# Optimization experiments

Hardware: AMD Instinct MI355X
Metric: run time of the kernel (lower is better)

## Reference

```python
import jax, jax.numpy as jnp
import numpy as np

WIN = 7       # window_size (square)
SHIFT = 3     # shift_size
HEADS = 4
WS = WIN * WIN  # 49 tokens per window


def _rel_index():
    # Swin relative position index, shape (WS*WS,), static ints
    coords = np.stack(np.meshgrid(np.arange(WIN), np.arange(WIN), indexing='ij'))
    cf = coords.reshape(2, -1)
    rel = (cf[:, :, None] - cf[:, None, :]).transpose(1, 2, 0)  # (WS, WS, 2)
    rel[:, :, 0] += WIN - 1
    rel[:, :, 1] += WIN - 1
    rel[:, :, 0] *= 2 * WIN - 1
    return rel.sum(-1).reshape(-1)

_REL_IDX = jnp.asarray(_rel_index())


def _attn_mask(H, W):
    # shift mask per window, shape (num_windows, WS, WS), static
    m = np.zeros((H, W), np.float32)
    cnt = 0
    for h in ((0, -WIN), (-WIN, -SHIFT), (-SHIFT, None)):
        for w in ((0, -WIN), (-WIN, -SHIFT), (-SHIFT, None)):
            m[h[0]:h[1], w[0]:w[1]] = cnt
            cnt += 1
    m = m.reshape(H // WIN, WIN, W // WIN, WIN).transpose(0, 2, 1, 3).reshape(-1, WS)
    diff = m[:, None, :] - m[:, :, None]
    return np.where(diff == 0, 0.0, -100.0).astype(np.float32)


def setup_inputs() -> dict:
    key = jax.random.key(0)
    ks = jax.random.split(key, 6)
    C = 128
    return {
        'x': jax.random.normal(ks[0], (64, 56, 56, C), jnp.float32),
        'qkv_kernel': jax.random.normal(ks[1], (C, 3 * C), jnp.float32) * (C ** -0.5),
        'qkv_bias': jax.random.normal(ks[2], (3 * C,), jnp.float32) * 0.02,
        'proj_kernel': jax.random.normal(ks[3], (C, C), jnp.float32) * (C ** -0.5),
        'proj_bias': jax.random.normal(ks[4], (C,), jnp.float32) * 0.02,
        'rel_pos_table': jax.random.normal(ks[5], ((2 * WIN - 1) ** 2, HEADS), jnp.float32) * 0.02,
    }


def reference(x, qkv_kernel, qkv_bias, proj_kernel, proj_bias, rel_pos_table):
    B, H, W, C = x.shape
    nH, nW = H // WIN, W // WIN
    head_dim = C // HEADS

    # cyclic shift + window partition -> (B*nH*nW, WS, C)
    xs = jnp.roll(x, (-SHIFT, -SHIFT), axis=(1, 2))
    xw = xs.reshape(B, nH, WIN, nW, WIN, C).transpose(0, 1, 3, 2, 4, 5).reshape(B * nH * nW, WS, C)

    qkv = xw @ qkv_kernel + qkv_bias
    qkv = qkv.reshape(-1, WS, 3, HEADS, head_dim).transpose(2, 0, 3, 1, 4)  # (3, n, h, WS, d)
    q, k, v = qkv[0], qkv[1], qkv[2]

    attn = jnp.einsum('nhsd,nhtd->nhst', q * head_dim ** -0.5, k)

    # relative position bias: (1, heads, WS, WS)
    bias = rel_pos_table[_REL_IDX].reshape(WS, WS, HEADS).transpose(2, 0, 1)[None]
    attn = attn + bias

    # shift mask (static)
    mask = jnp.asarray(_attn_mask(H, W))  # (nH*nW, WS, WS)
    attn = attn.reshape(B, nH * nW, HEADS, WS, WS) + mask[None, :, None]
    attn = jax.nn.softmax(attn.reshape(-1, HEADS, WS, WS), axis=-1)

    out = jnp.einsum('nhst,nhtd->nhsd', attn, v).transpose(0, 2, 1, 3).reshape(-1, WS, C)
    out = out @ proj_kernel + proj_bias

    # window merge + reverse shift
    out = out.reshape(B, nH, nW, WIN, WIN, C).transpose(0, 1, 3, 2, 4, 5).reshape(B, H, W, C)
    return jnp.roll(out, (SHIFT, SHIFT), axis=(1, 2))
```

## Files before the change

### kernel.cpp

```cpp
#include <hip/hip_runtime.h>
#include <hip/hip_bf16.h>

#define WIN 7
#define SHIFT_SZ 3
#define WSQ 49
#define CH 128
#define HW 56
#define LOG2E 1.4426950408889634f
#define QSCALE (0.17677669529663687f * LOG2E)

typedef short s16x8 __attribute__((ext_vector_type(8)));
typedef short s16x4 __attribute__((ext_vector_type(4)));
typedef float f32x4 __attribute__((ext_vector_type(4)));


__global__ void prep_weights(const float* __restrict__ qkv_kernel,
                             const float* __restrict__ proj_kernel,
                             __hip_bfloat16* __restrict__ ws) {
  int idx = blockIdx.x * 256 + threadIdx.x;
  if (idx < 49152) {
    int n = idx >> 7, c = idx & 127;
    ws[idx] = __float2bfloat16(qkv_kernel[c * 384 + n]);
  }
  if (idx < 16384) {
    int n = idx >> 7, c = idx & 127;
    ws[49152 + idx] = __float2bfloat16(proj_kernel[c * 128 + n]);
  }
}

__global__ void prep_tbl(const float* __restrict__ rel_pos_table,
                         __hip_bfloat16* __restrict__ tbl) {
  int idx = blockIdx.x * 256 + threadIdx.x;
  int t = idx & 63;
  int s = (idx >> 6) & 63;
  int h = (idx >> 12) & 3;
  int cls = idx >> 14;
  float v;
  if (t >= WSQ) v = -43280.f;
  else if (s >= WSQ) v = 0.f;
  else {
    int i1 = s / 7, j1 = s % 7, i2 = t / 7, j2 = t % 7;
    int ridx = (i1 - i2 + 6) * 13 + (j1 - j2 + 6);
    float bias = rel_pos_table[ridx * 4 + h];
    int wyIs7 = cls >> 1, wxIs7 = cls & 1;
    int rh1 = wyIs7 ? (i1 < 4 ? 1 : 2) : 0;
    int rh2 = wyIs7 ? (i2 < 4 ? 1 : 2) : 0;
    int rw1 = wxIs7 ? (j1 < 4 ? 1 : 2) : 0;
    int rw2 = wxIs7 ? (j2 < 4 ? 1 : 2) : 0;
    float mask = (rh1 == rh2 && rw1 == rw2) ? 0.f : -100.f;
    v = (bias + mask) * LOG2E;
  }
  tbl[idx] = __float2bfloat16(v);
}


__launch_bounds__(512, 6)
__global__ void swin_attn(const float* __restrict__ x,
                          const float* __restrict__ qkv_bias,
                          const float* __restrict__ proj_bias,
                          const __hip_bfloat16* __restrict__ wqkvT,
                          const __hip_bfloat16* __restrict__ wprojT,
                          const __hip_bfloat16* __restrict__ tbl,
                          float* __restrict__ out) {
  __shared__ __align__(16) char smem[49152];
  __hip_bfloat16* a_lds  = (__hip_bfloat16*)smem;
  __hip_bfloat16* q_lds  = (__hip_bfloat16*)smem;
  __hip_bfloat16* k_lds  = (__hip_bfloat16*)(smem + 16384);
  __hip_bfloat16* vt_lds = (__hip_bfloat16*)(smem + 32768);
  __hip_bfloat16* p_lds  = (__hip_bfloat16*)smem;
  __hip_bfloat16* o_lds  = (__hip_bfloat16*)(smem + 32768);

  const int tid = threadIdx.x;
  const int lane = tid & 63;
  const int wv = tid >> 6;
  const int g = lane >> 4;
  const int c = lane & 15;
  const int e = c & 7;
  const int e2 = (c >> 1) & 7;

  const int widx = blockIdx.x;
  const int b  = widx >> 6;
  const int wy = (widx >> 3) & 7;
  const int wx = widx & 7;
  const int mc = ((wy == 7) ? 2 : 0) + ((wx == 7) ? 1 : 0);

  for (int it = tid; it < 1024; it += 512) {
    int s = it >> 4;
    int l16 = it & 15;
    union { s16x8 v; __hip_bfloat16 h[8]; } u;
    if (s < WSQ) {
      int i = s / 7, j = s - i * 7;
      int hh = wy * 7 + i + SHIFT_SZ; if (hh >= HW) hh -= HW;
      int ww = wx * 7 + j + SHIFT_SZ; if (ww >= HW) ww -= HW;
      const float4* src = (const float4*)(x + (((b * HW + hh) * HW + ww) * CH + l16 * 8));
      float4 f0 = src[0], f1 = src[1];
      u.h[0] = __float2bfloat16(f0.x); u.h[1] = __float2bfloat16(f0.y);
      u.h[2] = __float2bfloat16(f0.z); u.h[3] = __float2bfloat16(f0.w);
      u.h[4] = __float2bfloat16(f1.x); u.h[5] = __float2bfloat16(f1.y);
      u.h[6] = __float2bfloat16(f1.z); u.h[7] = __float2bfloat16(f1.w);
    } else {
      #pragma unroll
      for (int q = 0; q < 8; ++q) u.h[q] = __float2bfloat16(0.f);
    }
    *(s16x8*)(a_lds + s * 128 + ((l16 ^ (s & 7)) * 8)) = u.v;
  }
  __syncthreads();

  {
    f32x4 acc_v[4];
    #pragma unroll
    for (int mt = 0; mt < 4; ++mt) acc_v[mt] = (f32x4){0.f, 0.f, 0.f, 0.f};
    #pragma unroll
    for (int kt = 0; kt < 4; ++kt) {
      s16x8 bv = *(const s16x8*)(wqkvT + (16 * (16 + wv) + c) * 128 + kt * 32 + g * 8);
      #pragma unroll
      for (int mt = 0; mt < 4; ++mt) {
        s16x8 af = *(const s16x8*)(a_lds + (16 * mt + c) * 128 + ((4 * kt + g) ^ e) * 8);
        acc_v[mt] = __builtin_amdgcn_mfma_f32_16x16x32_bf16(af, bv, acc_v[mt], 0, 0, 0);
      }
    }
    int hv = wv >> 1;
    int d = (wv & 1) * 16 + c;
    float bvb = qkv_bias[256 + wv * 16 + c];
    __hip_bfloat16* vdst = vt_lds + (hv * 32 + d) * 64;
    #pragma unroll
    for (int mt = 0; mt < 4; ++mt) {
      union { s16x4 v; __hip_bfloat16 h[4]; } u;
      #pragma unroll
      for (int r = 0; r < 4; ++r) u.h[r] = __float2bfloat16(acc_v[mt][r] + bvb);
      *(s16x4*)(vdst + ((2 * mt + (g >> 1)) ^ e) * 8 + (g & 1) * 4) = u.v;
    }
  }

  {
    f32x4 acc[2][4];
    #pragma unroll
    for (int ntl = 0; ntl < 2; ++ntl)
      #pragma unroll
      for (int mt = 0; mt < 4; ++mt) acc[ntl][mt] = (f32x4){0.f, 0.f, 0.f, 0.f};
    #pragma unroll
    for (int kt = 0; kt < 4; ++kt) {
      s16x8 af[4];
      #pragma unroll
      for (int mt = 0; mt < 4; ++mt)
        af[mt] = *(const s16x8*)(a_lds + (16 * mt + c) * 128 + ((4 * kt + g) ^ e) * 8);
      #pragma unroll
      for (int ntl = 0; ntl < 2; ++ntl) {
        s16x8 bf = *(const s16x8*)(wqkvT + (16 * (2 * wv + ntl) + c) * 128 + kt * 32 + g * 8);
        #pragma unroll
        for (int mt = 0; mt < 4; ++mt)
          acc[ntl][mt] = __builtin_amdgcn_mfma_f32_16x16x32_bf16(bf, af[mt], acc[ntl][mt], 0, 0, 0);
      }
    }
    const float scale = (wv < 4) ? QSCALE : 1.0f;
    if (wv >= 4) {
      #pragma unroll
      for (int ntl = 0; ntl < 2; ++ntl) {
        int qt = 2 * wv + ntl;
        int h = (qt >> 1) & 3;
        int blk = (qt & 1) * 4 + g;
        float4 b4 = *(const float4*)(qkv_bias + qt * 16 + 4 * g);
        __hip_bfloat16* dst = k_lds + h * 2048;
        #pragma unroll
        for (int mt = 0; mt < 4; ++mt) {
          union { s16x4 v; __hip_bfloat16 h[4]; } u;
          u.h[0] = __float2bfloat16((acc[ntl][mt][0] + b4.x) * scale);
          u.h[1] = __float2bfloat16((acc[ntl][mt][1] + b4.y) * scale);
          u.h[2] = __float2bfloat16((acc[ntl][mt][2] + b4.z) * scale);
          u.h[3] = __float2bfloat16((acc[ntl][mt][3] + b4.w) * scale);
          *(s16x4*)(dst + (16 * mt + c) * 32 + ((blk ^ e2) * 4)) = u.v;
        }
      }
    }
    __syncthreads();
    if (wv < 4) {
      #pragma unroll
      for (int ntl = 0; ntl < 2; ++ntl) {
        int qt = 2 * wv + ntl;
        int h = (qt >> 1) & 3;
        int blk = (qt & 1) * 4 + g;
        float4 b4 = *(const float4*)(qkv_bias + qt * 16 + 4 * g);
        __hip_bfloat16* dst = q_lds + h * 2048;
        #pragma unroll
        for (int mt = 0; mt < 4; ++mt) {
          union { s16x4 v; __hip_bfloat16 h[4]; } u;
          u.h[0] = __float2bfloat16((acc[ntl][mt][0] + b4.x) * scale);
          u.h[1] = __float2bfloat16((acc[ntl][mt][1] + b4.y) * scale);
          u.h[2] = __float2bfloat16((acc[ntl][mt][2] + b4.z) * scale);
          u.h[3] = __float2bfloat16((acc[ntl][mt][3] + b4.w) * scale);
          *(s16x4*)(dst + (16 * mt + c) * 32 + ((blk ^ e2) * 4)) = u.v;
        }
      }
    }
  }
  __syncthreads();

  const int h3 = wv >> 1;
  const int mh = wv & 1;
  s16x8 qf[2], kf[4];
  #pragma unroll
  for (int m = 0; m < 2; ++m) {
    const __hip_bfloat16* base = q_lds + h3 * 2048 + (16 * (2 * mh + m) + c) * 32;
    *(s16x4*)&qf[m] = *(const s16x4*)(base + ((2 * g) ^ e2) * 4);
    *(((s16x4*)&qf[m]) + 1) = *(const s16x4*)(base + ((2 * g + 1) ^ e2) * 4);
  }
  #pragma unroll
  for (int nt = 0; nt < 4; ++nt) {
    const __hip_bfloat16* base = k_lds + h3 * 2048 + (16 * nt + c) * 32;
    *(s16x4*)&kf[nt] = *(const s16x4*)(base + ((2 * g) ^ e2) * 4);
    *(((s16x4*)&kf[nt]) + 1) = *(const s16x4*)(base + ((2 * g + 1) ^ e2) * 4);
  }
  __syncthreads();

  #pragma unroll
  for (int m = 0; m < 2; ++m) {
    f32x4 sc[4];
    #pragma unroll
    for (int nt = 0; nt < 4; ++nt) {
      sc[nt] = (f32x4){0.f, 0.f, 0.f, 0.f};
      sc[nt] = __builtin_amdgcn_mfma_f32_16x16x32_bf16(kf[nt], qf[m], sc[nt], 0, 0, 0);
    }
    const __hip_bfloat16* tb_ =
        tbl + (((mc << 2) + h3) << 12) + (32 * mh + 16 * m + c) * 64;
    #pragma unroll
    for (int nt = 0; nt < 4; ++nt) {
      union { s16x4 v; __hip_bfloat16 h[4]; } tv;
      tv.v = *(const s16x4*)(tb_ + 16 * nt + 4 * g);
      #pragma unroll
      for (int r = 0; r < 4; ++r) sc[nt][r] += __bfloat162float(tv.h[r]);
    }
    float mx = -1e30f;
    #pragma unroll
    for (int nt = 0; nt < 4; ++nt)
      #pragma unroll
      for (int r = 0; r < 4; ++r) mx = fmaxf(mx, sc[nt][r]);
    mx = fmaxf(mx, __shfl_xor(mx, 16));
    mx = fmaxf(mx, __shfl_xor(mx, 32));
    float sum = 0.f;
    #pragma unroll
    for (int nt = 0; nt < 4; ++nt)
      #pragma unroll
      for (int r = 0; r < 4; ++r) {
        float e2f = __builtin_amdgcn_exp2f(sc[nt][r] - mx);
        sc[nt][r] = e2f;
        sum += e2f;
      }
    sum += __shfl_xor(sum, 16);
    sum += __shfl_xor(sum, 32);
    float inv = __builtin_amdgcn_rcpf(sum);
    __hip_bfloat16* prow = p_lds + (h3 * 64 + 16 * (2 * mh + m) + c) * 64;
    #pragma unroll
    for (int nt = 0; nt < 4; ++nt) {
      union { s16x4 v; __hip_bfloat16 h[4]; } u;
      #pragma unroll
      for (int r = 0; r < 4; ++r) u.h[r] = __float2bfloat16(sc[nt][r] * inv);
      *(s16x4*)(prow + ((2 * nt + (g >> 1)) ^ e) * 8 + (g & 1) * 4) = u.v;
    }
  }

  f32x4 oacc[2][2];
  #pragma unroll
  for (int m = 0; m < 2; ++m)
    #pragma unroll
    for (int ntd = 0; ntd < 2; ++ntd) oacc[m][ntd] = (f32x4){0.f, 0.f, 0.f, 0.f};
  #pragma unroll
  for (int kt = 0; kt < 2; ++kt) {
    s16x8 vfr[2], pfr[2];
    #pragma unroll
    for (int ntd = 0; ntd < 2; ++ntd)
      vfr[ntd] = *(const s16x8*)(vt_lds + (h3 * 32 + 16 * ntd + c) * 64 +
                                 (((4 * kt + g) ^ e) * 8));
    #pragma unroll
    for (int m = 0; m < 2; ++m)
      pfr[m] = *(const s16x8*)(p_lds + (h3 * 64 + 16 * (2 * mh + m) + c) * 64 +
                               (((4 * kt + g) ^ e) * 8));
    #pragma unroll
    for (int m = 0; m < 2; ++m)
      #pragma unroll
      for (int ntd = 0; ntd < 2; ++ntd)
        oacc[m][ntd] = __builtin_amdgcn_mfma_f32_16x16x32_bf16(vfr[ntd], pfr[m], oacc[m][ntd], 0, 0, 0);
  }
  __syncthreads();

  #pragma unroll
  for (int m = 0; m < 2; ++m)
    #pragma unroll
    for (int ntd = 0; ntd < 2; ++ntd) {
      union { s16x4 v; __hip_bfloat16 h[4]; } u;
      #pragma unroll
      for (int r = 0; r < 4; ++r) u.h[r] = __float2bfloat16(oacc[m][ntd][r]);
      *(s16x4*)(o_lds + (32 * mh + 16 * m + c) * 128 +
                ((4 * h3 + 2 * ntd + (g >> 1)) ^ e) * 8 + (g & 1) * 4) = u.v;
    }
  __syncthreads();

  {
    f32x4 pacc[4];
    #pragma unroll
    for (int mt = 0; mt < 4; ++mt) pacc[mt] = (f32x4){0.f, 0.f, 0.f, 0.f};
    #pragma unroll
    for (int kt = 0; kt < 4; ++kt) {
      s16x8 bfp = *(const s16x8*)(wprojT + (16 * wv + c) * 128 + kt * 32 + g * 8);
      #pragma unroll
      for (int mt = 0; mt < 4; ++mt) {
        s16x8 afo = *(const s16x8*)(o_lds + (16 * mt + c) * 128 + ((4 * kt + g) ^ e) * 8);
        pacc[mt] = __builtin_amdgcn_mfma_f32_16x16x32_bf16(bfp, afo, pacc[mt], 0, 0, 0);
      }
    }
    float4 pb4 = *(const float4*)(proj_bias + 16 * wv + 4 * g);
    #pragma unroll
    for (int mt = 0; mt < 4; ++mt) {
      int s = 16 * mt + c;
      if (s < WSQ) {
        int i = s / 7, j = s - i * 7;
        int hh = wy * 7 + i + SHIFT_SZ; if (hh >= HW) hh -= HW;
        int ww = wx * 7 + j + SHIFT_SZ; if (ww >= HW) ww -= HW;
        float4 v;
        v.x = pacc[mt][0] + pb4.x;
        v.y = pacc[mt][1] + pb4.y;
        v.z = pacc[mt][2] + pb4.z;
        v.w = pacc[mt][3] + pb4.w;
        *(float4*)(out + ((b * HW + hh) * HW + ww) * CH + 16 * wv + 4 * g) = v;
      }
    }
  }
}

extern "C" void kernel_launch(void* const* d_in, const int* in_sizes, int n_in,
                              void* d_out, int out_size, void* d_ws, size_t ws_size,
                              hipStream_t stream) {
  const float* x            = (const float*)d_in[0];
  const float* qkv_kernel   = (const float*)d_in[1];
  const float* qkv_bias     = (const float*)d_in[2];
  const float* proj_kernel  = (const float*)d_in[3];
  const float* proj_bias    = (const float*)d_in[4];
  const float* rel_pos_tbl  = (const float*)d_in[5];
  float* out = (float*)d_out;

  __hip_bfloat16* wsb    = (__hip_bfloat16*)d_ws;
  __hip_bfloat16* wqkvT  = wsb;
  __hip_bfloat16* wprojT = wsb + 49152;
  __hip_bfloat16* tbl    = wsb + 65536;

  prep_weights<<<dim3(192), dim3(256), 0, stream>>>(qkv_kernel, proj_kernel, wsb);
  prep_tbl<<<dim3(256), dim3(256), 0, stream>>>(rel_pos_tbl, tbl);
  swin_attn<<<dim3(4096), dim3(512), 0, stream>>>(x, qkv_bias, proj_bias,
                                                  wqkvT, wprojT, tbl, out);
}
```

Measured before the change: 133.0 us.

## Keep Q in registers, fold scale into weights, defer softmax normalization

Folds the QK scale into the Q weights and bias during weight prep, and seeds the accumulators with the biases so no separate bias add is needed. Each wave now computes only the Q rows it consumes and keeps them in registers as 16x16x16 MFMA operands, so Q no longer goes through LDS and one barrier phase is removed. The relative-position table values seed the score accumulators, and softmax normalization moves to after the PV product, which shrinks the multiply work. The risks are higher register pressure and redundant Q projection work across waves that share rows.

```diff
diff --git a/kernel.cpp b/kernel.cpp
--- a/kernel.cpp
+++ b/kernel.cpp
@@ -13,18 +13,35 @@
 typedef short s16x4 __attribute__((ext_vector_type(4)));
 typedef float f32x4 __attribute__((ext_vector_type(4)));
 
+static __device__ __forceinline__ f32x4 mfma16(s16x4 a, s16x4 b, f32x4 c) {
+#if __has_builtin(__builtin_amdgcn_mfma_f32_16x16x16bf16_1k)
+  return __builtin_amdgcn_mfma_f32_16x16x16bf16_1k(a, b, c, 0, 0, 0);
+#else
+  f32x4 d;
+  asm("v_mfma_f32_16x16x16_bf16 %0, %1, %2, %3" : "=v"(d) : "v"(a), "v"(b), "v"(c));
+  return d;
+#endif
+}
+
 
 __global__ void prep_weights(const float* __restrict__ qkv_kernel,
                              const float* __restrict__ proj_kernel,
+                             const float* __restrict__ qkv_bias,
                              __hip_bfloat16* __restrict__ ws) {
   int idx = blockIdx.x * 256 + threadIdx.x;
   if (idx < 49152) {
     int n = idx >> 7, c = idx & 127;
-    ws[idx] = __float2bfloat16(qkv_kernel[c * 384 + n]);
+    float w = qkv_kernel[c * 384 + n];
+    if (n < 128) w *= QSCALE;
+    ws[idx] = __float2bfloat16(w);
   }
   if (idx < 16384) {
     int n = idx >> 7, c = idx & 127;
     ws[49152 + idx] = __float2bfloat16(proj_kernel[c * 128 + n]);
+  }
+  if (idx < 384) {
+    float* bf = (float*)(ws + 131072);
+    bf[idx] = qkv_bias[idx] * (idx < 128 ? QSCALE : 1.0f);
   }
 }
 
@@ -56,7 +73,7 @@
 
 __launch_bounds__(512, 6)
 __global__ void swin_attn(const float* __restrict__ x,
-                          const float* __restrict__ qkv_bias,
+                          const float* __restrict__ biasf,
                           const float* __restrict__ proj_bias,
                           const __hip_bfloat16* __restrict__ wqkvT,
                           const __hip_bfloat16* __restrict__ wprojT,
@@ -64,7 +81,6 @@
                           float* __restrict__ out) {
   __shared__ __align__(16) char smem[49152];
   __hip_bfloat16* a_lds  = (__hip_bfloat16*)smem;
-  __hip_bfloat16* q_lds  = (__hip_bfloat16*)smem;
   __hip_bfloat16* k_lds  = (__hip_bfloat16*)(smem + 16384);
   __hip_bfloat16* vt_lds = (__hip_bfloat16*)(smem + 32768);
   __hip_bfloat16* p_lds  = (__hip_bfloat16*)smem;
@@ -83,6 +99,9 @@
   const int wy = (widx >> 3) & 7;
   const int wx = widx & 7;
   const int mc = ((wy == 7) ? 2 : 0) + ((wx == 7) ? 1 : 0);
+
+  const int h3 = wv >> 1;
+  const int mh = wv & 1;
 
   for (int it = tid; it < 1024; it += 512) {
     int s = it >> 4;
@@ -107,127 +126,115 @@
   __syncthreads();
 
   {
-    f32x4 acc_v[4];
-    #pragma unroll
-    for (int mt = 0; mt < 4; ++mt) acc_v[mt] = (f32x4){0.f, 0.f, 0.f, 0.f};
+    float4 kb4 = *(const float4*)(biasf + 128 + 16 * wv + 4 * g);
+    f32x4 acc[4];
+    #pragma unroll
+    for (int mt = 0; mt < 4; ++mt) acc[mt] = (f32x4){kb4.x, kb4.y, kb4.z, kb4.w};
     #pragma unroll
     for (int kt = 0; kt < 4; ++kt) {
-      s16x8 bv = *(const s16x8*)(wqkvT + (16 * (16 + wv) + c) * 128 + kt * 32 + g * 8);
+      s16x8 bf = *(const s16x8*)(wqkvT + (128 + 16 * wv + c) * 128 + kt * 32 + g * 8);
       #pragma unroll
       for (int mt = 0; mt < 4; ++mt) {
         s16x8 af = *(const s16x8*)(a_lds + (16 * mt + c) * 128 + ((4 * kt + g) ^ e) * 8);
-        acc_v[mt] = __builtin_amdgcn_mfma_f32_16x16x32_bf16(af, bv, acc_v[mt], 0, 0, 0);
+        acc[mt] = __builtin_amdgcn_mfma_f32_16x16x32_bf16(bf, af, acc[mt], 0, 0, 0);
+      }
+    }
+    __hip_bfloat16* dst = k_lds + (wv >> 1) * 2048;
+    int blk = ((wv & 1) * 4 + g) ^ e2;
+    #pragma unroll
+    for (int mt = 0; mt < 4; ++mt) {
+      union { s16x4 v; __hip_bfloat16 h[4]; } u;
+      #pragma unroll
+      for (int r = 0; r < 4; ++r) u.h[r] = __float2bfloat16(acc[mt][r]);
+      *(s16x4*)(dst + (16 * mt + c) * 32 + blk * 4) = u.v;
+    }
+  }
+
+  {
+    float bvb = biasf[256 + 16 * wv + c];
+    f32x4 acc[4];
+    #pragma unroll
+    for (int mt = 0; mt < 4; ++mt) acc[mt] = (f32x4){bvb, bvb, bvb, bvb};
+    #pragma unroll
+    for (int kt = 0; kt < 4; ++kt) {
+      s16x8 bv = *(const s16x8*)(wqkvT + (256 + 16 * wv + c) * 128 + kt * 32 + g * 8);
+      #pragma unroll
+      for (int mt = 0; mt < 4; ++mt) {
+        s16x8 af = *(const s16x8*)(a_lds + (16 * mt + c) * 128 + ((4 * kt + g) ^ e) * 8);
+        acc[mt] = __builtin_amdgcn_mfma_f32_16x16x32_bf16(af, bv, acc[mt], 0, 0, 0);
       }
     }
     int hv = wv >> 1;
     int d = (wv & 1) * 16 + c;
-    float bvb = qkv_bias[256 + wv * 16 + c];
     __hip_bfloat16* vdst = vt_lds + (hv * 32 + d) * 64;
     #pragma unroll
     for (int mt = 0; mt < 4; ++mt) {
       union { s16x4 v; __hip_bfloat16 h[4]; } u;
       #pragma unroll
-      for (int r = 0; r < 4; ++r) u.h[r] = __float2bfloat16(acc_v[mt][r] + bvb);
+      for (int r = 0; r < 4; ++r) u.h[r] = __float2bfloat16(acc[mt][r]);
       *(s16x4*)(vdst + ((2 * mt + (g >> 1)) ^ e) * 8 + (g & 1) * 4) = u.v;
     }
   }
 
+  s16x4 qf16[2][2];
   {
-    f32x4 acc[2][4];
-    #pragma unroll
-    for (int ntl = 0; ntl < 2; ++ntl)
-      #pragma unroll
-      for (int mt = 0; mt < 4; ++mt) acc[ntl][mt] = (f32x4){0.f, 0.f, 0.f, 0.f};
+    f32x4 acc[2][2];
+    #pragma unroll
+    for (int kb = 0; kb < 2; ++kb) {
+      float4 qb4 = *(const float4*)(biasf + 32 * h3 + 16 * kb + 4 * g);
+      #pragma unroll
+      for (int m = 0; m < 2; ++m) acc[kb][m] = (f32x4){qb4.x, qb4.y, qb4.z, qb4.w};
+    }
     #pragma unroll
     for (int kt = 0; kt < 4; ++kt) {
-      s16x8 af[4];
-      #pragma unroll
-      for (int mt = 0; mt < 4; ++mt)
-        af[mt] = *(const s16x8*)(a_lds + (16 * mt + c) * 128 + ((4 * kt + g) ^ e) * 8);
-      #pragma unroll
-      for (int ntl = 0; ntl < 2; ++ntl) {
-        s16x8 bf = *(const s16x8*)(wqkvT + (16 * (2 * wv + ntl) + c) * 128 + kt * 32 + g * 8);
+      s16x8 afq[2];
+      #pragma unroll
+      for (int m = 0; m < 2; ++m)
+        afq[m] = *(const s16x8*)(a_lds + (16 * (2 * mh + m) + c) * 128 + ((4 * kt + g) ^ e) * 8);
+      #pragma unroll
+      for (int kb = 0; kb < 2; ++kb) {
+        s16x8 bf = *(const s16x8*)(wqkvT + (32 * h3 + 16 * kb + c) * 128 + kt * 32 + g * 8);
         #pragma unroll
-        for (int mt = 0; mt < 4; ++mt)
-          acc[ntl][mt] = __builtin_amdgcn_mfma_f32_16x16x32_bf16(bf, af[mt], acc[ntl][mt], 0, 0, 0);
-      }
-    }
-    const float scale = (wv < 4) ? QSCALE : 1.0f;
-    if (wv >= 4) {
-      #pragma unroll
-      for (int ntl = 0; ntl < 2; ++ntl) {
-        int qt = 2 * wv + ntl;
-        int h = (qt >> 1) & 3;
-        int blk = (qt & 1) * 4 + g;
-        float4 b4 = *(const float4*)(qkv_bias + qt * 16 + 4 * g);
-        __hip_bfloat16* dst = k_lds + h * 2048;
+        for (int m = 0; m < 2; ++m)
+          acc[kb][m] = __builtin_amdgcn_mfma_f32_16x16x32_bf16(bf, afq[m], acc[kb][m], 0, 0, 0);
+      }
+    }
+    #pragma unroll
+    for (int kb = 0; kb < 2; ++kb)
+      #pragma unroll
+      for (int m = 0; m < 2; ++m) {
+        union { s16x4 v; __hip_bfloat16 h[4]; } u;
         #pragma unroll
-        for (int mt = 0; mt < 4; ++mt) {
-          union { s16x4 v; __hip_bfloat16 h[4]; } u;
-          u.h[0] = __float2bfloat16((acc[ntl][mt][0] + b4.x) * scale);
-          u.h[1] = __float2bfloat16((acc[ntl][mt][1] + b4.y) * scale);
-          u.h[2] = __float2bfloat16((acc[ntl][mt][2] + b4.z) * scale);
-          u.h[3] = __float2bfloat16((acc[ntl][mt][3] + b4.w) * scale);
-          *(s16x4*)(dst + (16 * mt + c) * 32 + ((blk ^ e2) * 4)) = u.v;
-        }
-      }
-    }
-    __syncthreads();
-    if (wv < 4) {
-      #pragma unroll
-      for (int ntl = 0; ntl < 2; ++ntl) {
-        int qt = 2 * wv + ntl;
-        int h = (qt >> 1) & 3;
-        int blk = (qt & 1) * 4 + g;
-        float4 b4 = *(const float4*)(qkv_bias + qt * 16 + 4 * g);
-        __hip_bfloat16* dst = q_lds + h * 2048;
-        #pragma unroll
-        for (int mt = 0; mt < 4; ++mt) {
-          union { s16x4 v; __hip_bfloat16 h[4]; } u;
-          u.h[0] = __float2bfloat16((acc[ntl][mt][0] + b4.x) * scale);
-          u.h[1] = __float2bfloat16((acc[ntl][mt][1] + b4.y) * scale);
-          u.h[2] = __float2bfloat16((acc[ntl][mt][2] + b4.z) * scale);
-          u.h[3] = __float2bfloat16((acc[ntl][mt][3] + b4.w) * scale);
-          *(s16x4*)(dst + (16 * mt + c) * 32 + ((blk ^ e2) * 4)) = u.v;
-        }
-      }
-    }
-  }
-  __syncthreads();
-
-  const int h3 = wv >> 1;
-  const int mh = wv & 1;
-  s16x8 qf[2], kf[4];
+        for (int r = 0; r < 4; ++r) u.h[r] = __float2bfloat16(acc[kb][m][r]);
+        qf16[kb][m] = u.v;
+      }
+  }
+  __syncthreads();
+
+  s16x4 kf16[2][4];
+  #pragma unroll
+  for (int kb = 0; kb < 2; ++kb)
+    #pragma unroll
+    for (int nt = 0; nt < 4; ++nt)
+      kf16[kb][nt] = *(const s16x4*)(k_lds + h3 * 2048 + (16 * nt + c) * 32 +
+                                     (((4 * kb + g) ^ e2) * 4));
+  __syncthreads();
+
+  float inv[2];
   #pragma unroll
   for (int m = 0; m < 2; ++m) {
-    const __hip_bfloat16* base = q_lds + h3 * 2048 + (16 * (2 * mh + m) + c) * 32;
-    *(s16x4*)&qf[m] = *(const s16x4*)(base + ((2 * g) ^ e2) * 4);
-    *(((s16x4*)&qf[m]) + 1) = *(const s16x4*)(base + ((2 * g + 1) ^ e2) * 4);
-  }
-  #pragma unroll
-  for (int nt = 0; nt < 4; ++nt) {
-    const __hip_bfloat16* base = k_lds + h3 * 2048 + (16 * nt + c) * 32;
-    *(s16x4*)&kf[nt] = *(const s16x4*)(base + ((2 * g) ^ e2) * 4);
-    *(((s16x4*)&kf[nt]) + 1) = *(const s16x4*)(base + ((2 * g + 1) ^ e2) * 4);
-  }
-  __syncthreads();
-
-  #pragma unroll
-  for (int m = 0; m < 2; ++m) {
-    f32x4 sc[4];
-    #pragma unroll
-    for (int nt = 0; nt < 4; ++nt) {
-      sc[nt] = (f32x4){0.f, 0.f, 0.f, 0.f};
-      sc[nt] = __builtin_amdgcn_mfma_f32_16x16x32_bf16(kf[nt], qf[m], sc[nt], 0, 0, 0);
-    }
     const __hip_bfloat16* tb_ =
         tbl + (((mc << 2) + h3) << 12) + (32 * mh + 16 * m + c) * 64;
+    f32x4 sc[4];
     #pragma unroll
     for (int nt = 0; nt < 4; ++nt) {
       union { s16x4 v; __hip_bfloat16 h[4]; } tv;
       tv.v = *(const s16x4*)(tb_ + 16 * nt + 4 * g);
       #pragma unroll
-      for (int r = 0; r < 4; ++r) sc[nt][r] += __bfloat162float(tv.h[r]);
+      for (int r = 0; r < 4; ++r) sc[nt][r] = __bfloat162float(tv.h[r]);
+      #pragma unroll
+      for (int kb = 0; kb < 2; ++kb)
+        sc[nt] = mfma16(kf16[kb][nt], qf16[kb][m], sc[nt]);
     }
     float mx = -1e30f;
     #pragma unroll
@@ -241,21 +248,21 @@
     for (int nt = 0; nt < 4; ++nt)
       #pragma unroll
       for (int r = 0; r < 4; ++r) {
-        float e2f = __builtin_amdgcn_exp2f(sc[nt][r] - mx);
-        sc[nt][r] = e2f;
-        sum += e2f;
-      }
+        float ex = __builtin_amdgcn_exp2f(sc[nt][r] - mx);
+        sc[nt][r] = ex;
+        sum += ex;
+      }
+    __hip_bfloat16* prow = p_lds + (h3 * 64 + 16 * (2 * mh + m) + c) * 64;
+    #pragma unroll
+    for (int nt = 0; nt < 4; ++nt) {
+      union { s16x4 v; __hip_bfloat16 h[4]; } u;
+      #pragma unroll
+      for (int r = 0; r < 4; ++r) u.h[r] = __float2bfloat16(sc[nt][r]);
+      *(s16x4*)(prow + ((2 * nt + (g >> 1)) ^ e) * 8 + (g & 1) * 4) = u.v;
+    }
     sum += __shfl_xor(sum, 16);
     sum += __shfl_xor(sum, 32);
-    float inv = __builtin_amdgcn_rcpf(sum);
-    __hip_bfloat16* prow = p_lds + (h3 * 64 + 16 * (2 * mh + m) + c) * 64;
-    #pragma unroll
-    for (int nt = 0; nt < 4; ++nt) {
-      union { s16x4 v; __hip_bfloat16 h[4]; } u;
-      #pragma unroll
-      for (int r = 0; r < 4; ++r) u.h[r] = __float2bfloat16(sc[nt][r] * inv);
-      *(s16x4*)(prow + ((2 * nt + (g >> 1)) ^ e) * 8 + (g & 1) * 4) = u.v;
-    }
+    inv[m] = __builtin_amdgcn_rcpf(sum);
   }
 
   f32x4 oacc[2][2];
@@ -288,16 +295,17 @@
     for (int ntd = 0; ntd < 2; ++ntd) {
       union { s16x4 v; __hip_bfloat16 h[4]; } u;
       #pragma unroll
-      for (int r = 0; r < 4; ++r) u.h[r] = __float2bfloat16(oacc[m][ntd][r]);
+      for (int r = 0; r < 4; ++r) u.h[r] = __float2bfloat16(oacc[m][ntd][r] * inv[m]);
       *(s16x4*)(o_lds + (32 * mh + 16 * m + c) * 128 +
                 ((4 * h3 + 2 * ntd + (g >> 1)) ^ e) * 8 + (g & 1) * 4) = u.v;
     }
   __syncthreads();
 
   {
+    float4 pb4 = *(const float4*)(proj_bias + 16 * wv + 4 * g);
     f32x4 pacc[4];
     #pragma unroll
-    for (int mt = 0; mt < 4; ++mt) pacc[mt] = (f32x4){0.f, 0.f, 0.f, 0.f};
+    for (int mt = 0; mt < 4; ++mt) pacc[mt] = (f32x4){pb4.x, pb4.y, pb4.z, pb4.w};
     #pragma unroll
     for (int kt = 0; kt < 4; ++kt) {
       s16x8 bfp = *(const s16x8*)(wprojT + (16 * wv + c) * 128 + kt * 32 + g * 8);
@@ -307,7 +315,6 @@
         pacc[mt] = __builtin_amdgcn_mfma_f32_16x16x32_bf16(bfp, afo, pacc[mt], 0, 0, 0);
       }
     }
-    float4 pb4 = *(const float4*)(proj_bias + 16 * wv + 4 * g);
     #pragma unroll
     for (int mt = 0; mt < 4; ++mt) {
       int s = 16 * mt + c;
@@ -316,10 +323,10 @@
         int hh = wy * 7 + i + SHIFT_SZ; if (hh >= HW) hh -= HW;
         int ww = wx * 7 + j + SHIFT_SZ; if (ww >= HW) ww -= HW;
         float4 v;
-        v.x = pacc[mt][0] + pb4.x;
-        v.y = pacc[mt][1] + pb4.y;
-        v.z = pacc[mt][2] + pb4.z;
-        v.w = pacc[mt][3] + pb4.w;
+        v.x = pacc[mt][0];
+        v.y = pacc[mt][1];
+        v.z = pacc[mt][2];
+        v.w = pacc[mt][3];
         *(float4*)(out + ((b * HW + hh) * HW + ww) * CH + 16 * wv + 4 * g) = v;
       }
     }
@@ -341,9 +348,11 @@
   __hip_bfloat16* wqkvT  = wsb;
   __hip_bfloat16* wprojT = wsb + 49152;
   __hip_bfloat16* tbl    = wsb + 65536;
-
-  prep_weights<<<dim3(192), dim3(256), 0, stream>>>(qkv_kernel, proj_kernel, wsb);
+  const float* biasf     = (const float*)(wsb + 131072);
+
+  prep_weights<<<dim3(192), dim3(256), 0, stream>>>(qkv_kernel, proj_kernel,
+                                                    qkv_bias, wsb);
   prep_tbl<<<dim3(256), dim3(256), 0, stream>>>(rel_pos_tbl, tbl);
-  swin_attn<<<dim3(4096), dim3(512), 0, stream>>>(x, qkv_bias, proj_bias,
+  swin_attn<<<dim3(4096), dim3(512), 0, stream>>>(x, biasf, proj_bias,
                                                   wqkvT, wprojT, tbl, out);
 }
```

Result: slower. 140.6 us (+5.7%).
